# Performance work log

Measured on AMD Instinct MI355X. Metric: run time of the kernel, lower is better.

## Reference

```python
import jax, jax.numpy as jnp
import numpy as np

N = 12288
IN_C = 64
OUT_C = 64
NEG_INF = -1.0e9

def setup_inputs() -> dict:
    key = jax.random.key(0)
    k1, k2, k3, k4 = jax.random.split(key, 4)
    x = jax.random.normal(k1, (N, IN_C), dtype=jnp.float32)
    edge_index = jax.random.randint(k2, (N, N), 0, 2, dtype=jnp.int32)
    # xavier-ish scaling for params
    weight_w = jax.random.normal(k3, (IN_C, OUT_C), dtype=jnp.float32) * (1.0 / np.sqrt(IN_C))
    weight_a = jax.random.normal(k4, (2 * OUT_C, 1), dtype=jnp.float32) * (1.0 / np.sqrt(OUT_C))
    bias = jnp.zeros((OUT_C,), dtype=jnp.float32)
    return {"x": x, "edge_index": edge_index, "weight_w": weight_w,
            "weight_a": weight_a, "bias": bias}

def reference(x, edge_index, weight_w, weight_a, bias):
    wh = x @ weight_w                              # [N, out]
    a_src = weight_a[:OUT_C, 0]                    # [out]
    a_dst = weight_a[OUT_C:, 0]                    # [out]
    # rank-1 additive score: e[i,j] = <wh_i, a_src> + <wh_j, a_dst>
    e = (wh @ a_src)[:, None] + (wh @ a_dst)[None, :]   # [N, N]
    e = jax.nn.leaky_relu(e, negative_slope=0.01)        # torch LeakyReLU default
    scores = jnp.where(edge_index > 0, e, NEG_INF)
    attention = jax.nn.softmax(scores, axis=1)           # row-wise
    out = attention @ wh                                  # [N, out]
    return out + bias
```

## Files before the change

kernel.cpp:

```cpp
#include <hip/hip_runtime.h>
#include <hip/hip_bf16.h>
#include <cstddef>
#include <cstdint>

#define Nn 12288

typedef __bf16 bf16x8 __attribute__((ext_vector_type(8)));
typedef float  f32x4  __attribute__((ext_vector_type(4)));
typedef int    i32x4  __attribute__((ext_vector_type(4)));

__device__ __forceinline__ void gload_lds16(const void* g, void* l) {
    __builtin_amdgcn_global_load_lds(
        (const __attribute__((address_space(1))) void*)g,
        (__attribute__((address_space(3))) void*)l, 16, 0, 0);
}

__global__ __launch_bounds__(256) void prep_kernel(
    const float* __restrict__ x, const float* __restrict__ W,
    const float* __restrict__ wa, __bf16* __restrict__ whB,
    float* __restrict__ src, float* __restrict__ dst)
{
    __shared__ float  Wl[64 * 64];
    __shared__ float  Xl[64 * 64];
    __shared__ __bf16 whl[64 * 72];
    int t = threadIdx.x;
    int R0 = blockIdx.x * 64;
    for (int i = t; i < 4096; i += 256) {
        Wl[i] = W[i];
        Xl[i] = x[(size_t)R0 * 64 + i];
    }
    __syncthreads();
    int c   = t & 63;
    int r16 = (t >> 6) * 16;
    float vals[16];
    #pragma unroll
    for (int k = 0; k < 16; ++k) vals[k] = 0.f;
    #pragma unroll 16
    for (int kk = 0; kk < 64; ++kk) {
        float wv = Wl[kk * 64 + c];
        #pragma unroll
        for (int k = 0; k < 16; ++k)
            vals[k] = fmaf(Xl[(r16 + k) * 64 + kk], wv, vals[k]);
    }
    #pragma unroll
    for (int k = 0; k < 16; ++k) whl[c * 72 + r16 + k] = (__bf16)vals[k];
    __syncthreads();
    if (t < 64) {
        float s = 0.f, d = 0.f;
        #pragma unroll 16
        for (int cc = 0; cc < 64; ++cc) {
            float v = (float)whl[cc * 72 + t];
            s = fmaf(v, wa[cc], s);
            d = fmaf(v, wa[64 + cc], d);
        }
        src[R0 + t] = s;
        dst[R0 + t] = d;
    }
    #pragma unroll
    for (int gg = 0; gg < 2; ++gg) {
        int gidx   = t * 2 + gg;
        int jc_loc = gidx >> 8;
        int q      = (gidx >> 6) & 3;
        int lane   = gidx & 63;
        int crow   = (lane & 15) + 16 * q;
        int jrow   = jc_loc * 32 + (lane >> 4) * 8;
        bf16x8 v = *(const bf16x8*)&whl[crow * 72 + jrow];
        int jc = blockIdx.x * 2 + jc_loc;
        *(bf16x8*)&whB[((size_t)(jc * 4 + q) * 64 + lane) * 8] = v;
    }
}

__device__ __forceinline__ void chunk_mfma(
    float srow, i32x4 m0, i32x4 m1, f32x4 d0, f32x4 d1,
    bf16x8 b0, bf16x8 b1, bf16x8 b2, bf16x8 b3,
    f32x4& a0, f32x4& a1, f32x4& a2, f32x4& a3, float& zacc)
{
    bf16x8 pa;
    #pragma unroll
    for (int e = 0; e < 4; ++e) {
        float t0 = srow + d0[e];
        float f0 = fmaxf(t0, 0.01f * t0);
        float w0 = __expf(f0);
        w0 = (m0[e] > 0) ? w0 : 0.f;
        zacc += w0;
        pa[e] = (__bf16)w0;
        float t1 = srow + d1[e];
        float f1 = fmaxf(t1, 0.01f * t1);
        float w1 = __expf(f1);
        w1 = (m1[e] > 0) ? w1 : 0.f;
        zacc += w1;
        pa[4 + e] = (__bf16)w1;
    }
    a0 = __builtin_amdgcn_mfma_f32_16x16x32_bf16(pa, b0, a0, 0, 0, 0);
    a1 = __builtin_amdgcn_mfma_f32_16x16x32_bf16(pa, b1, a1, 0, 0, 0);
    a2 = __builtin_amdgcn_mfma_f32_16x16x32_bf16(pa, b2, a2, 0, 0, 0);
    a3 = __builtin_amdgcn_mfma_f32_16x16x32_bf16(pa, b3, a3, 0, 0, 0);
}

template <int NSEG>
__global__ __launch_bounds__(256, 4) void attn_kernel(
    const int* __restrict__ mask, const __bf16* __restrict__ whB,
    const float* __restrict__ src, const float* __restrict__ dstv,
    float* __restrict__ pnum, float* __restrict__ pz)
{
    constexpr int NT = (Nn / NSEG) / 256;
    __shared__ int lm[2 * 16 * 260];

    int t    = threadIdx.x;
    int lane = t & 63;
    int wid  = t >> 6;
    int g    = blockIdx.x / NSEG;
    int seg  = blockIdx.x % NSEG;
    int row  = lane & 15;
    int kg   = lane >> 4;
    int segbase = seg * (Nn / NSEG);
    float srow = src[g * 16 + row];

#define STAGE(b, tt)                                                          \
    do {                                                                      \
        _Pragma("unroll")                                                     \
        for (int rr = 0; rr < 4; ++rr) {                                      \
            int rs = wid * 4 + rr;                                            \
            const int* gp = mask + (size_t)(g * 16 + rs) * Nn + segbase +     \
                            (tt) * 256 + lane * 4;                            \
            gload_lds16(gp, &lm[(b) * 4160 + rs * 260]);                      \
        }                                                                     \
    } while (0)

    int cur = 0;
    STAGE(0, 0);
    f32x4 acc0 = {0.f, 0.f, 0.f, 0.f}, acc1 = acc0, acc2 = acc0, acc3 = acc0;
    float zacc = 0.f;

    for (int tt = 0; tt < NT; ++tt) {
        int jt = segbase + tt * 256 + wid * 64;
        int jl = kg * 8;
        f32x4 d00 = *(const f32x4*)(dstv + jt + jl);
        f32x4 d01 = *(const f32x4*)(dstv + jt + jl + 4);
        f32x4 d10 = *(const f32x4*)(dstv + jt + 32 + jl);
        f32x4 d11 = *(const f32x4*)(dstv + jt + 32 + jl + 4);
        size_t jc0 = (size_t)(jt >> 5);
        const __bf16* wb0 = whB + (jc0 * 4) * 512 + lane * 8;
        const __bf16* wb1 = whB + ((jc0 + 1) * 4) * 512 + lane * 8;
        bf16x8 b00 = *(const bf16x8*)(wb0);
        bf16x8 b01 = *(const bf16x8*)(wb0 + 512);
        bf16x8 b02 = *(const bf16x8*)(wb0 + 1024);
        bf16x8 b03 = *(const bf16x8*)(wb0 + 1536);
        bf16x8 b10 = *(const bf16x8*)(wb1);
        bf16x8 b11 = *(const bf16x8*)(wb1 + 512);
        bf16x8 b12 = *(const bf16x8*)(wb1 + 1024);
        bf16x8 b13 = *(const bf16x8*)(wb1 + 1536);
        __builtin_amdgcn_sched_barrier(0);
        if (tt + 1 < NT) {
            STAGE(cur ^ 1, tt + 1);
            asm volatile("s_waitcnt vmcnt(4)" ::: "memory");
        } else {
            asm volatile("s_waitcnt vmcnt(0)" ::: "memory");
        }
        __builtin_amdgcn_sched_barrier(0);
        __builtin_amdgcn_s_barrier();
        const int* mbase = &lm[cur * 4160];
        i32x4 m00 = *(const i32x4*)&mbase[row * 260 + wid * 64 + jl];
        i32x4 m01 = *(const i32x4*)&mbase[row * 260 + wid * 64 + jl + 4];
        i32x4 m10 = *(const i32x4*)&mbase[row * 260 + wid * 64 + 32 + jl];
        i32x4 m11 = *(const i32x4*)&mbase[row * 260 + wid * 64 + 32 + jl + 4];
        chunk_mfma(srow, m00, m01, d00, d01, b00, b01, b02, b03,
                   acc0, acc1, acc2, acc3, zacc);
        chunk_mfma(srow, m10, m11, d10, d11, b10, b11, b12, b13,
                   acc0, acc1, acc2, acc3, zacc);
        __builtin_amdgcn_s_barrier();
        cur ^= 1;
    }
#undef STAGE

    float* red  = (float*)lm;
    float* redz = red + 4096;
    #pragma unroll
    for (int r = 0; r < 4; ++r) {
        int orow = kg * 4 + r;
        red[wid * 1024 + orow * 64 + row]      = acc0[r];
        red[wid * 1024 + orow * 64 + row + 16] = acc1[r];
        red[wid * 1024 + orow * 64 + row + 32] = acc2[r];
        red[wid * 1024 + orow * 64 + row + 48] = acc3[r];
    }
    zacc += __shfl_xor(zacc, 16);
    zacc += __shfl_xor(zacc, 32);
    if (lane < 16) redz[wid * 16 + lane] = zacc;
    __syncthreads();
    #pragma unroll
    for (int k = 0; k < 4; ++k) {
        int idx = k * 256 + t;
        float sv = red[idx] + red[1024 + idx] + red[2048 + idx] + red[3072 + idx];
        pnum[(size_t)seg * Nn * 64 + (size_t)g * 1024 + idx] = sv;
    }
    if (t < 16)
        pz[(size_t)seg * Nn + g * 16 + t] =
            redz[t] + redz[16 + t] + redz[32 + t] + redz[48 + t];
}

__global__ __launch_bounds__(256) void finalize_kernel(
    const float* __restrict__ pnum, const float* __restrict__ pz,
    const float* __restrict__ bias, float* __restrict__ out, int nseg)
{
    int idx = blockIdx.x * 256 + threadIdx.x;
    int i = idx >> 6, c = idx & 63;
    float num = 0.f, z = 0.f;
    for (int s = 0; s < nseg; ++s) {
        num += pnum[(size_t)s * Nn * 64 + idx];
        z   += pz[(size_t)s * Nn + i];
    }
    z = (z != 0.f) ? z : 1.f;
    out[idx] = num / z + bias[c];
}

extern "C" void kernel_launch(void* const* d_in, const int* in_sizes, int n_in,
                              void* d_out, int out_size, void* d_ws, size_t ws_size,
                              hipStream_t stream) {
    const float* x    = (const float*)d_in[0];
    const int*   mask = (const int*)d_in[1];
    const float* W    = (const float*)d_in[2];
    const float* wa   = (const float*)d_in[3];
    const float* bias = (const float*)d_in[4];
    float* out = (float*)d_out;

    char* ws = (char*)d_ws;
    const size_t whB_bytes = (size_t)Nn * 64 * 2;
    const size_t vec_bytes = (size_t)Nn * 4;
    __bf16* whB = (__bf16*)ws;
    float*  src = (float*)(ws + whB_bytes);
    float*  dst = (float*)(ws + whB_bytes + vec_bytes);
    size_t fixed = whB_bytes + 2 * vec_bytes;
    size_t per_seg = (size_t)Nn * 64 * 4 + (size_t)Nn * 4;

    int nseg = 4;
    while (nseg > 1 && fixed + (size_t)nseg * per_seg > ws_size) nseg >>= 1;

    float* pnum = (float*)(ws + fixed);
    float* pz   = (float*)(ws + fixed + (size_t)nseg * Nn * 64 * 4);

    prep_kernel<<<Nn / 64, 256, 0, stream>>>(x, W, wa, whB, src, dst);

    int blocks = 768 * nseg;
    switch (nseg) {
        case 4: attn_kernel<4><<<blocks, 256, 0, stream>>>(mask, whB, src, dst, pnum, pz); break;
        case 2: attn_kernel<2><<<blocks, 256, 0, stream>>>(mask, whB, src, dst, pnum, pz); break;
        default: attn_kernel<1><<<blocks, 256, 0, stream>>>(mask, whB, src, dst, pnum, pz); break;
    }

    finalize_kernel<<<(Nn * 64) / 256, 256, 0, stream>>>(pnum, pz, bias, out, nseg);
}
```

Measured before the change: 166.9 us.

## Drop split-K segments, fuse finalize into attention kernel, prefetch B operands one tile ahead

Removes the column-segment split and the separate finalize kernel, so each 16-row block walks the full 12288 columns and writes normalized output plus bias directly. The whB operands are now loaded one tile ahead with inline asm into a double-buffered register set, dst values are staged into LDS alongside the mask, and mask loads use a non-temporal cache hint. The LDS row stride also changes. This removes partial-sum traffic and a kernel launch, but cuts the grid from 3072 to 768 blocks, which risks lower occupancy and less latency hiding. Register pressure also rises with the 16-vector prefetch buffer.

```diff
diff --git a/kernel.cpp b/kernel.cpp
--- a/kernel.cpp
+++ b/kernel.cpp
@@ -4,15 +4,23 @@
 #include <cstdint>
 
 #define Nn 12288
+#define NTIL 48
+#define MSTRIDE 264
+#define DSTOFF (2 * 16 * MSTRIDE)
 
 typedef __bf16 bf16x8 __attribute__((ext_vector_type(8)));
 typedef float  f32x4  __attribute__((ext_vector_type(4)));
 typedef int    i32x4  __attribute__((ext_vector_type(4)));
 
-__device__ __forceinline__ void gload_lds16(const void* g, void* l) {
+__device__ __forceinline__ void gload_lds16_nt(const void* g, void* l) {
     __builtin_amdgcn_global_load_lds(
         (const __attribute__((address_space(1))) void*)g,
-        (__attribute__((address_space(3))) void*)l, 16, 0, 0);
+        (__attribute__((address_space(3))) void*)l, 16, 0, 2 );
+}
+__device__ __forceinline__ void gload_lds4(const void* g, void* l) {
+    __builtin_amdgcn_global_load_lds(
+        (const __attribute__((address_space(1))) void*)g,
+        (__attribute__((address_space(3))) void*)l, 4, 0, 0);
 }
 
 __global__ __launch_bounds__(256) void prep_kernel(
@@ -70,109 +78,136 @@
     }
 }
 
-__device__ __forceinline__ void chunk_mfma(
-    float srow, i32x4 m0, i32x4 m1, f32x4 d0, f32x4 d1,
-    bf16x8 b0, bf16x8 b1, bf16x8 b2, bf16x8 b3,
-    f32x4& a0, f32x4& a1, f32x4& a2, f32x4& a3, float& zacc)
-{
-    bf16x8 pa;
-    #pragma unroll
-    for (int e = 0; e < 4; ++e) {
-        float t0 = srow + d0[e];
-        float f0 = fmaxf(t0, 0.01f * t0);
-        float w0 = __expf(f0);
-        w0 = (m0[e] > 0) ? w0 : 0.f;
-        zacc += w0;
-        pa[e] = (__bf16)w0;
-        float t1 = srow + d1[e];
-        float f1 = fmaxf(t1, 0.01f * t1);
-        float w1 = __expf(f1);
-        w1 = (m1[e] > 0) ? w1 : 0.f;
-        zacc += w1;
-        pa[4 + e] = (__bf16)w1;
-    }
-    a0 = __builtin_amdgcn_mfma_f32_16x16x32_bf16(pa, b0, a0, 0, 0, 0);
-    a1 = __builtin_amdgcn_mfma_f32_16x16x32_bf16(pa, b1, a1, 0, 0, 0);
-    a2 = __builtin_amdgcn_mfma_f32_16x16x32_bf16(pa, b2, a2, 0, 0, 0);
-    a3 = __builtin_amdgcn_mfma_f32_16x16x32_bf16(pa, b3, a3, 0, 0, 0);
-}
-
-template <int NSEG>
-__global__ __launch_bounds__(256, 4) void attn_kernel(
+__global__ __launch_bounds__(256) void attn_kernel(
     const int* __restrict__ mask, const __bf16* __restrict__ whB,
     const float* __restrict__ src, const float* __restrict__ dstv,
-    float* __restrict__ pnum, float* __restrict__ pz)
+    const float* __restrict__ bias, float* __restrict__ out)
 {
-    constexpr int NT = (Nn / NSEG) / 256;
-    __shared__ int lm[2 * 16 * 260];
+    __shared__ int lm[DSTOFF + 2 * 256];
 
     int t    = threadIdx.x;
     int lane = t & 63;
     int wid  = t >> 6;
-    int g    = blockIdx.x / NSEG;
-    int seg  = blockIdx.x % NSEG;
+    int g    = blockIdx.x;
     int row  = lane & 15;
     int kg   = lane >> 4;
-    int segbase = seg * (Nn / NSEG);
+    int jl   = kg * 8;
+
     float srow = src[g * 16 + row];
-
-#define STAGE(b, tt)                                                          \
+    asm volatile("" :: "v"(srow));
+
+    i32x4 bset[2][8];
+    f32x4 acc0 = {0.f, 0.f, 0.f, 0.f}, acc1 = acc0, acc2 = acc0, acc3 = acc0;
+    float zacc = 0.f;
+
+#define STAGE(B, TT)                                                          \
     do {                                                                      \
         _Pragma("unroll")                                                     \
         for (int rr = 0; rr < 4; ++rr) {                                      \
             int rs = wid * 4 + rr;                                            \
-            const int* gp = mask + (size_t)(g * 16 + rs) * Nn + segbase +     \
-                            (tt) * 256 + lane * 4;                            \
-            gload_lds16(gp, &lm[(b) * 4160 + rs * 260]);                      \
+            gload_lds16_nt(mask + (size_t)(g * 16 + rs) * Nn + (TT) * 256 +   \
+                               lane * 4,                                      \
+                           &lm[(B) * 4224 + rs * MSTRIDE]);                   \
         }                                                                     \
-    } while (0)
-
-    int cur = 0;
+        gload_lds4(dstv + (TT) * 256 + wid * 64 + lane,                       \
+                   &lm[DSTOFF + (B) * 256 + wid * 64]);                       \
+    } while (0)
+
+#define BLOAD(P, TT)                                                          \
+    do {                                                                      \
+        const char* _b0 = (const char*)whB +                                  \
+                          ((size_t)((TT) * 8 + wid * 2)) * 4096 +             \
+                          (size_t)lane * 16;                                  \
+        const char* _b1 = _b0 + 4096;                                         \
+        asm volatile("global_load_dwordx4 %0, %1, off"                        \
+                     : "=v"(bset[P][0]) : "v"(_b0));                          \
+        asm volatile("global_load_dwordx4 %0, %1, off offset:1024"            \
+                     : "=v"(bset[P][1]) : "v"(_b0));                          \
+        asm volatile("global_load_dwordx4 %0, %1, off offset:2048"            \
+                     : "=v"(bset[P][2]) : "v"(_b0));                          \
+        asm volatile("global_load_dwordx4 %0, %1, off offset:3072"            \
+                     : "=v"(bset[P][3]) : "v"(_b0));                          \
+        asm volatile("global_load_dwordx4 %0, %1, off"                        \
+                     : "=v"(bset[P][4]) : "v"(_b1));                          \
+        asm volatile("global_load_dwordx4 %0, %1, off offset:1024"            \
+                     : "=v"(bset[P][5]) : "v"(_b1));                          \
+        asm volatile("global_load_dwordx4 %0, %1, off offset:2048"            \
+                     : "=v"(bset[P][6]) : "v"(_b1));                          \
+        asm volatile("global_load_dwordx4 %0, %1, off offset:3072"            \
+                     : "=v"(bset[P][7]) : "v"(_b1));                          \
+    } while (0)
+
+#define COMPUTE(TT, B, P)                                                     \
+    do {                                                                      \
+        const int*   mb = &lm[(B) * 4224 + row * MSTRIDE + wid * 64];         \
+        const float* db = (const float*)&lm[DSTOFF + (B) * 256 + wid * 64];   \
+        _Pragma("unroll")                                                     \
+        for (int cc = 0; cc < 2; ++cc) {                                      \
+            i32x4 m0 = *(const i32x4*)(mb + cc * 32 + jl);                    \
+            i32x4 m1 = *(const i32x4*)(mb + cc * 32 + jl + 4);                \
+            f32x4 d0 = *(const f32x4*)(db + cc * 32 + jl);                    \
+            f32x4 d1 = *(const f32x4*)(db + cc * 32 + jl + 4);                \
+            bf16x8 pa;                                                        \
+            _Pragma("unroll")                                                 \
+            for (int e = 0; e < 4; ++e) {                                     \
+                float t0 = srow + d0[e];                                      \
+                float f0 = fmaxf(t0, 0.01f * t0);                             \
+                float w0 = __expf(f0);                                        \
+                w0 = (m0[e] > 0) ? w0 : 0.f;                                  \
+                zacc += w0;                                                   \
+                pa[e] = (__bf16)w0;                                           \
+                float t1 = srow + d1[e];                                      \
+                float f1 = fmaxf(t1, 0.01f * t1);                             \
+                float w1 = __expf(f1);                                        \
+                w1 = (m1[e] > 0) ? w1 : 0.f;                                  \
+                zacc += w1;                                                   \
+                pa[4 + e] = (__bf16)w1;                                       \
+            }                                                                 \
+            acc0 = __builtin_amdgcn_mfma_f32_16x16x32_bf16(                   \
+                pa, __builtin_bit_cast(bf16x8, bset[P][cc * 4 + 0]), acc0, 0, 0, 0); \
+            acc1 = __builtin_amdgcn_mfma_f32_16x16x32_bf16(                   \
+                pa, __builtin_bit_cast(bf16x8, bset[P][cc * 4 + 1]), acc1, 0, 0, 0); \
+            acc2 = __builtin_amdgcn_mfma_f32_16x16x32_bf16(                   \
+                pa, __builtin_bit_cast(bf16x8, bset[P][cc * 4 + 2]), acc2, 0, 0, 0); \
+            acc3 = __builtin_amdgcn_mfma_f32_16x16x32_bf16(                   \
+                pa, __builtin_bit_cast(bf16x8, bset[P][cc * 4 + 3]), acc3, 0, 0, 0); \
+        }                                                                     \
+    } while (0)
+
+#define BODY_FULL(P)                                                          \
+    do {                                                                      \
+        STAGE((P) ^ 1, tt + 1);                                               \
+        BLOAD((P) ^ 1, tt + 1);                                               \
+        asm volatile("s_waitcnt vmcnt(13)" ::: "memory");                     \
+        __builtin_amdgcn_sched_barrier(0);                                    \
+        __builtin_amdgcn_s_barrier();                                         \
+        __builtin_amdgcn_sched_barrier(0);                                    \
+        COMPUTE(tt, P, P);                                                    \
+        __builtin_amdgcn_s_barrier();                                         \
+        ++tt;                                                                 \
+    } while (0)
+
+    int tt = 0;
     STAGE(0, 0);
-    f32x4 acc0 = {0.f, 0.f, 0.f, 0.f}, acc1 = acc0, acc2 = acc0, acc3 = acc0;
-    float zacc = 0.f;
-
-    for (int tt = 0; tt < NT; ++tt) {
-        int jt = segbase + tt * 256 + wid * 64;
-        int jl = kg * 8;
-        f32x4 d00 = *(const f32x4*)(dstv + jt + jl);
-        f32x4 d01 = *(const f32x4*)(dstv + jt + jl + 4);
-        f32x4 d10 = *(const f32x4*)(dstv + jt + 32 + jl);
-        f32x4 d11 = *(const f32x4*)(dstv + jt + 32 + jl + 4);
-        size_t jc0 = (size_t)(jt >> 5);
-        const __bf16* wb0 = whB + (jc0 * 4) * 512 + lane * 8;
-        const __bf16* wb1 = whB + ((jc0 + 1) * 4) * 512 + lane * 8;
-        bf16x8 b00 = *(const bf16x8*)(wb0);
-        bf16x8 b01 = *(const bf16x8*)(wb0 + 512);
-        bf16x8 b02 = *(const bf16x8*)(wb0 + 1024);
-        bf16x8 b03 = *(const bf16x8*)(wb0 + 1536);
-        bf16x8 b10 = *(const bf16x8*)(wb1);
-        bf16x8 b11 = *(const bf16x8*)(wb1 + 512);
-        bf16x8 b12 = *(const bf16x8*)(wb1 + 1024);
-        bf16x8 b13 = *(const bf16x8*)(wb1 + 1536);
-        __builtin_amdgcn_sched_barrier(0);
-        if (tt + 1 < NT) {
-            STAGE(cur ^ 1, tt + 1);
-            asm volatile("s_waitcnt vmcnt(4)" ::: "memory");
-        } else {
-            asm volatile("s_waitcnt vmcnt(0)" ::: "memory");
-        }
-        __builtin_amdgcn_sched_barrier(0);
-        __builtin_amdgcn_s_barrier();
-        const int* mbase = &lm[cur * 4160];
-        i32x4 m00 = *(const i32x4*)&mbase[row * 260 + wid * 64 + jl];
-        i32x4 m01 = *(const i32x4*)&mbase[row * 260 + wid * 64 + jl + 4];
-        i32x4 m10 = *(const i32x4*)&mbase[row * 260 + wid * 64 + 32 + jl];
-        i32x4 m11 = *(const i32x4*)&mbase[row * 260 + wid * 64 + 32 + jl + 4];
-        chunk_mfma(srow, m00, m01, d00, d01, b00, b01, b02, b03,
-                   acc0, acc1, acc2, acc3, zacc);
-        chunk_mfma(srow, m10, m11, d10, d11, b10, b11, b12, b13,
-                   acc0, acc1, acc2, acc3, zacc);
-        __builtin_amdgcn_s_barrier();
-        cur ^= 1;
-    }
+    BLOAD(0, 0);
+
+    for (int it = 0; it < 23; ++it) {
+        BODY_FULL(0);
+        BODY_FULL(1);
+    }
+    BODY_FULL(0);
+    asm volatile("s_waitcnt vmcnt(0)" ::: "memory");
+    __builtin_amdgcn_sched_barrier(0);
+    __builtin_amdgcn_s_barrier();
+    __builtin_amdgcn_sched_barrier(0);
+    COMPUTE(47, 1, 1);
+
+#undef BODY_FULL
+#undef COMPUTE
+#undef BLOAD
 #undef STAGE
 
+    __syncthreads();
     float* red  = (float*)lm;
     float* redz = red + 4096;
     #pragma unroll
@@ -190,27 +225,12 @@
     #pragma unroll
     for (int k = 0; k < 4; ++k) {
         int idx = k * 256 + t;
+        int i   = idx >> 6;
         float sv = red[idx] + red[1024 + idx] + red[2048 + idx] + red[3072 + idx];
-        pnum[(size_t)seg * Nn * 64 + (size_t)g * 1024 + idx] = sv;
-    }
-    if (t < 16)
-        pz[(size_t)seg * Nn + g * 16 + t] =
-            redz[t] + redz[16 + t] + redz[32 + t] + redz[48 + t];
-}
-
-__global__ __launch_bounds__(256) void finalize_kernel(
-    const float* __restrict__ pnum, const float* __restrict__ pz,
-    const float* __restrict__ bias, float* __restrict__ out, int nseg)
-{
-    int idx = blockIdx.x * 256 + threadIdx.x;
-    int i = idx >> 6, c = idx & 63;
-    float num = 0.f, z = 0.f;
-    for (int s = 0; s < nseg; ++s) {
-        num += pnum[(size_t)s * Nn * 64 + idx];
-        z   += pz[(size_t)s * Nn + i];
-    }
-    z = (z != 0.f) ? z : 1.f;
-    out[idx] = num / z + bias[c];
+        float z  = redz[i] + redz[16 + i] + redz[32 + i] + redz[48 + i];
+        z = (z != 0.f) ? z : 1.f;
+        out[(size_t)g * 1024 + idx] = sv / z + bias[idx & 63];
+    }
 }
 
 extern "C" void kernel_launch(void* const* d_in, const int* in_sizes, int n_in,
@@ -229,23 +249,7 @@
     __bf16* whB = (__bf16*)ws;
     float*  src = (float*)(ws + whB_bytes);
     float*  dst = (float*)(ws + whB_bytes + vec_bytes);
-    size_t fixed = whB_bytes + 2 * vec_bytes;
-    size_t per_seg = (size_t)Nn * 64 * 4 + (size_t)Nn * 4;
-
-    int nseg = 4;
-    while (nseg > 1 && fixed + (size_t)nseg * per_seg > ws_size) nseg >>= 1;
-
-    float* pnum = (float*)(ws + fixed);
-    float* pz   = (float*)(ws + fixed + (size_t)nseg * Nn * 64 * 4);
 
     prep_kernel<<<Nn / 64, 256, 0, stream>>>(x, W, wa, whB, src, dst);
-
-    int blocks = 768 * nseg;
-    switch (nseg) {
-        case 4: attn_kernel<4><<<blocks, 256, 0, stream>>>(mask, whB, src, dst, pnum, pz); break;
-        case 2: attn_kernel<2><<<blocks, 256, 0, stream>>>(mask, whB, src, dst, pnum, pz); break;
-        default: attn_kernel<1><<<blocks, 256, 0, stream>>>(mask, whB, src, dst, pnum, pz); break;
-    }
-
-    finalize_kernel<<<(Nn * 64) / 256, 256, 0, stream>>>(pnum, pz, bias, out, nseg);
-}
+    attn_kernel<<<Nn / 16, 256, 0, stream>>>(mask, whB, src, dst, bias, out);
+}
```

Result: faster. 142.9 us (-14.4%).
